# Kernel tuning notes

Measured on AMD Instinct MI355X. Metric: run time of the kernel, lower is better.

The kernel has to match this reference:

```python
import jax, jax.numpy as jnp
import numpy as np

B, C, H, W = 4, 128, 64, 64
E, N, R, K = 256, 16, 8, 4   # d_inner=2C, d_state, dt_rank=ceil(C/16), conv kernel
L = H * W
EPS = 1e-5
NEG_SLOPE = 0.01


def setup_inputs() -> dict:
    key = jax.random.key(0)
    ks = jax.random.split(key, 8)
    p = {}
    p["x"] = jax.random.normal(ks[0], (B, C, H, W), jnp.float32)
    p["bn_gamma"] = jnp.ones((2, C), jnp.float32)
    p["bn_beta"] = jnp.zeros((2, C), jnp.float32)
    p["ln_gamma"] = jnp.ones((2, C), jnp.float32)
    p["ln_beta"] = jnp.zeros((2, C), jnp.float32)
    p["W_in"] = jax.random.normal(ks[1], (2, C, 2 * E), jnp.float32) * 0.02
    p["conv_w"] = jax.random.normal(ks[2], (2, E, K), jnp.float32) * 0.1
    p["conv_b"] = jnp.zeros((2, E), jnp.float32)
    p["W_xp"] = jax.random.normal(ks[3], (2, E, R + 2 * N), jnp.float32) * 0.02
    p["W_dt"] = jax.random.normal(ks[4], (2, R, E), jnp.float32) * 0.1
    # dt bias chosen so softplus(dt) is small/stable (mamba-style init)
    p["b_dt"] = jax.random.uniform(ks[5], (2, E), jnp.float32, minval=-4.0, maxval=-2.0)
    p["A_log"] = jnp.broadcast_to(jnp.log(jnp.arange(1, N + 1, dtype=jnp.float32)), (2, E, N)) + jnp.zeros((2, E, N), jnp.float32)
    p["Dp"] = jnp.ones((2, E), jnp.float32)
    p["W_out"] = jax.random.normal(ks[6], (2, E, C), jnp.float32) * 0.02
    return p


def _stage(x, i, bn_gamma, bn_beta, ln_gamma, ln_beta, W_in, conv_w, conv_b,
           W_xp, W_dt, b_dt, A_log, Dp, W_out):
    # --- BatchNorm2d (batch statistics, biased var, as torch training mode) ---
    mu = x.mean((0, 2, 3))
    var = x.var((0, 2, 3))
    xn = (x - mu[None, :, None, None]) * jax.lax.rsqrt(var + EPS)[None, :, None, None]
    xn = xn * bn_gamma[i][None, :, None, None] + bn_beta[i][None, :, None, None]
    # --- LeakyReLU ---
    xn = jax.nn.leaky_relu(xn, NEG_SLOPE)
    # --- SF_Block (Mamba S6 over L = H*W tokens) ---
    u = xn.transpose(0, 2, 3, 1).reshape(B, L, C)          # [B,L,C] tokens
    mu2 = u.mean(-1, keepdims=True)
    v2 = u.var(-1, keepdims=True)
    un = (u - mu2) * jax.lax.rsqrt(v2 + EPS) * ln_gamma[i] + ln_beta[i]
    xz = un @ W_in[i]                                       # [B,L,2E]
    xm, z = xz[..., :E], xz[..., E:]
    # causal depthwise conv1d along L
    xc = xm.transpose(0, 2, 1)                              # [B,E,L]
    xc = jax.lax.conv_general_dilated(xc, conv_w[i][:, None, :], (1,), [(K - 1, 0)],
                                      feature_group_count=E)
    xm = jax.nn.silu(xc.transpose(0, 2, 1) + conv_b[i])     # [B,L,E]
    dbl = xm @ W_xp[i]                                      # [B,L,R+2N]
    dt = jax.nn.softplus(dbl[..., :R] @ W_dt[i] + b_dt[i])  # [B,L,E]
    Bm = dbl[..., R:R + N]                                  # [B,L,N]
    Cm = dbl[..., R + N:]                                   # [B,L,N]
    A = -jnp.exp(A_log[i])                                  # [E,N]
    dA = jnp.exp(dt[..., None] * A)                         # [B,L,E,N]
    dBx = dt[..., None] * Bm[:, :, None, :] * xm[..., None] # [B,L,E,N]

    def step(h, inp):
        dA_t, dBx_t, C_t = inp
        h = dA_t * h + dBx_t                                # [B,E,N]
        y = jnp.einsum('ben,bn->be', h, C_t)
        return h, y

    h0 = jnp.zeros((B, E, N), xm.dtype)
    _, ys = jax.lax.scan(step, h0, (dA.transpose(1, 0, 2, 3),
                                    dBx.transpose(1, 0, 2, 3),
                                    Cm.transpose(1, 0, 2)))
    y = ys.transpose(1, 0, 2) + Dp[i] * xm                  # skip (D) term
    y = y * jax.nn.silu(z)                                  # gate
    out = y @ W_out[i]                                      # [B,L,C]
    out = u + out                                           # SF residual (drop_path=0)
    return out.reshape(B, H, W, C).transpose(0, 3, 1, 2)


def reference(x, bn_gamma, bn_beta, ln_gamma, ln_beta, W_in, conv_w, conv_b,
              W_xp, W_dt, b_dt, A_log, Dp, W_out):
    residual = x
    out = _stage(x, 0, bn_gamma, bn_beta, ln_gamma, ln_beta, W_in, conv_w, conv_b,
                 W_xp, W_dt, b_dt, A_log, Dp, W_out)
    out = _stage(out, 1, bn_gamma, bn_beta, ln_gamma, ln_beta, W_in, conv_w, conv_b,
                 W_xp, W_dt, b_dt, A_log, Dp, W_out)
    return out + residual
```

## Files before the change

### kernel.cpp

```cpp
#include <hip/hip_runtime.h>
#include <math.h>

#define Bc 4
#define Cc 128
#define Lc 4096
#define Ec 256
#define Nc 16
#define Rc 8
#define Kc 4
#define ROWS (Bc*Lc)
#define EPSc 1e-5f
#define SLOPE 0.01f

#define NCH 128
#define Tc 32
#define SC 16
#define SCL (NCH/SC)

typedef __attribute__((ext_vector_type(8))) short bf16x8;
typedef __attribute__((ext_vector_type(4))) float f32x4;

__device__ inline unsigned pack_bf16_2(float x, float y) {
    unsigned bx = __float_as_uint(x);
    unsigned by = __float_as_uint(y);
    bx = (bx + 0x7FFFu + ((bx >> 16) & 1u)) >> 16;
    by = (by + 0x7FFFu + ((by >> 16) & 1u)) & 0xFFFF0000u;
    return bx | by;
}
__device__ inline unsigned short to_bf16_rne(float x) {
    unsigned b = __float_as_uint(x);
    return (unsigned short)((b + 0x7FFFu + ((b >> 16) & 1u)) >> 16);
}
__device__ inline float bf16f(unsigned short u) {
    return __uint_as_float((unsigned)u << 16);
}
__device__ inline float sigmoidf_fast(float s) {
    return 1.f / (1.f + __expf(-s));
}
__device__ inline float softplusf(float s) {
    return fmaxf(s, 0.f) + __logf(1.f + __expf(-fabsf(s)));
}

__global__ void transpose_in(const float* __restrict__ x, float* __restrict__ xblc) {
    __shared__ float tile[32][33];
    int b = blockIdx.z;
    int l0 = blockIdx.x * 32, c0 = blockIdx.y * 32;
    int tx = threadIdx.x, ty = threadIdx.y;
    tile[ty][tx] = x[((size_t)(b * Cc + c0 + ty)) * Lc + l0 + tx];
    __syncthreads();
    xblc[((size_t)(b * Lc + l0 + ty)) * Cc + c0 + tx] = tile[tx][ty];
}

__device__ inline void wt_one(const float* W, unsigned short* Wt, int idx,
                              int K, int N, int NPAD) {
    int k = idx % K;
    int n = (idx / K) % NPAD;
    int i = idx / (K * NPAD);
    float v = (n < N) ? W[(size_t)i * K * N + (size_t)k * N + n] : 0.f;
    Wt[idx] = to_bf16_rne(v);
}
#define WT1 (2*512*128)
#define WT2 (2*64*256)
#define WT3 (2*128*256)
__global__ void wt_convert_all(const float* __restrict__ W_in, unsigned short* Wt_in,
                               const float* __restrict__ W_xp, unsigned short* Wt_xp,
                               const float* __restrict__ W_out, unsigned short* Wt_out) {
    int idx = blockIdx.x * 256 + threadIdx.x;
    if (idx < WT1) { wt_one(W_in, Wt_in, idx, 128, 512, 512); return; }
    idx -= WT1;
    if (idx < WT2) { wt_one(W_xp, Wt_xp, idx, 256, 40, 64); return; }
    idx -= WT2;
    if (idx < WT3) { wt_one(W_out, Wt_out, idx, 256, 128, 128); }
}

__global__ void bn_stats_partial(const float* __restrict__ xblc, float* __restrict__ part) {
    int c = threadIdx.x;
    int r0 = blockIdx.x * 64;
    float s = 0.f, s2 = 0.f;
    for (int r = 0; r < 64; r++) {
        float v = xblc[(size_t)(r0 + r) * Cc + c];
        s += v; s2 += v * v;
    }
    part[(size_t)blockIdx.x * 256 + c]       = s;
    part[(size_t)blockIdx.x * 256 + 128 + c] = s2;
}
__global__ void bn_stats_final(const float* __restrict__ part, float* __restrict__ sums) {
    int c = threadIdx.x;
    float s = 0.f, s2 = 0.f;
    for (int p = 0; p < 256; p++) {
        s  += part[(size_t)p * 256 + c];
        s2 += part[(size_t)p * 256 + 128 + c];
    }
    sums[c] = s;
    sums[128 + c] = s2;
}

__global__ __launch_bounds__(256) void bn_ln(
        const float* __restrict__ xin, const float* __restrict__ sums,
        const float* __restrict__ bng, const float* __restrict__ bnb,
        const float* __restrict__ lng, const float* __restrict__ lnb,
        float* __restrict__ un) {
    int wave = threadIdx.x >> 6, lane = threadIdx.x & 63;
    int row = blockIdx.x * 4 + wave;
    int c = lane * 2;
    float2 v = *(const float2*)(xin + (size_t)row * Cc + c);
    float2 sm = *(const float2*)(sums + c);
    float2 sq = *(const float2*)(sums + 128 + c);
    float2 g  = *(const float2*)(bng + c);
    float2 bt = *(const float2*)(bnb + c);
    const float inv = 1.f / (float)ROWS;
    float m0 = sm.x * inv, m1 = sm.y * inv;
    float va0 = sq.x * inv - m0 * m0, va1 = sq.y * inv - m1 * m1;
    float xn0 = (v.x - m0) * rsqrtf(va0 + EPSc) * g.x + bt.x;
    float xn1 = (v.y - m1) * rsqrtf(va1 + EPSc) * g.y + bt.y;
    xn0 = (xn0 < 0.f) ? SLOPE * xn0 : xn0;
    xn1 = (xn1 < 0.f) ? SLOPE * xn1 : xn1;
    float s = xn0 + xn1;
    float s2 = xn0 * xn0 + xn1 * xn1;
    #pragma unroll
    for (int m = 1; m < 64; m <<= 1) {
        s  += __shfl_xor(s, m, 64);
        s2 += __shfl_xor(s2, m, 64);
    }
    float m2 = s * (1.f / 128.f);
    float v2 = s2 * (1.f / 128.f) - m2 * m2;
    float rstd = rsqrtf(v2 + EPSc);
    float2 lg = *(const float2*)(lng + c);
    float2 lb = *(const float2*)(lnb + c);
    float2 o;
    o.x = (xn0 - m2) * rstd * lg.x + lb.x;
    o.y = (xn1 - m2) * rstd * lg.y + lb.y;
    *(float2*)(un + (size_t)row * Cc + c) = o;
}

__global__ __launch_bounds__(512) void fused_mid(
        const float* __restrict__ un,
        const unsigned short* __restrict__ Wt_in,
        const float* __restrict__ cw, const float* __restrict__ cb,
        const unsigned short* __restrict__ Wt_xp,
        const float* __restrict__ Wdt, const float* __restrict__ bdt,
        const float* __restrict__ Alog,
        unsigned short* __restrict__ zbuf,
        unsigned* __restrict__ dtxc,
        float* __restrict__ dbl,
        float2* __restrict__ PF) {
    __shared__ __align__(16) unsigned short xmtile[32][Ec + 8];
    __shared__ __align__(16) unsigned short dtt[32][Ec];
    __shared__ unsigned short xmprev[3][Ec];
    __shared__ float dblsh[32][40];
    __shared__ float d8[32][8];
    int tid = threadIdx.x;
    int wave = tid >> 6, lane = tid & 63;
    int quad = lane >> 4, l16 = lane & 15;
    int r0 = blockIdx.x * 32;
    int l0 = r0 & (Lc - 1);

    {
        int rt = wave >> 2;
        int cb4 = (wave & 3) * 8;
        const float* arow = un + (size_t)(r0 + rt * 16 + l16) * Cc + quad * 8;
        bf16x8 af[4];
        #pragma unroll
        for (int s = 0; s < 4; s++) {
            float4 a0 = *(const float4*)(arow + s * 32);
            float4 a1 = *(const float4*)(arow + s * 32 + 4);
            union { unsigned u[4]; bf16x8 v; } t;
            t.u[0] = pack_bf16_2(a0.x, a0.y);
            t.u[1] = pack_bf16_2(a0.z, a0.w);
            t.u[2] = pack_bf16_2(a1.x, a1.y);
            t.u[3] = pack_bf16_2(a1.z, a1.w);
            af[s] = t.v;
        }
        if (l0 != 0) {
            const float* hrow = un + (size_t)(r0 - 16 + l16) * Cc + quad * 8;
            bf16x8 hf[4];
            #pragma unroll
            for (int s = 0; s < 4; s++) {
                float4 a0 = *(const float4*)(hrow + s * 32);
                float4 a1 = *(const float4*)(hrow + s * 32 + 4);
                union { unsigned u[4]; bf16x8 v; } t;
                t.u[0] = pack_bf16_2(a0.x, a0.y);
                t.u[1] = pack_bf16_2(a0.z, a0.w);
                t.u[2] = pack_bf16_2(a1.x, a1.y);
                t.u[3] = pack_bf16_2(a1.z, a1.w);
                hf[s] = t.v;
            }
            #pragma unroll
            for (int c = 0; c < 2; c++) {
                int ct = wave * 2 + c;
                f32x4 acc = f32x4{0, 0, 0, 0};
                const unsigned short* bb = Wt_in + (size_t)(ct * 16 + l16) * Cc + quad * 8;
                #pragma unroll
                for (int s = 0; s < 4; s++)
                    acc = __builtin_amdgcn_mfma_f32_16x16x32_bf16(
                        hf[s], *(const bf16x8*)(bb + s * 32), acc, 0, 0, 0);
                #pragma unroll
                for (int r = 0; r < 4; r++) {
                    int rr = quad * 4 + r;
                    if (rr >= 13) xmprev[rr - 13][ct * 16 + l16] = to_bf16_rne(acc[r]);
                }
            }
        } else {
            for (int idx = tid; idx < 3 * Ec; idx += 512)
                xmprev[idx / Ec][idx % Ec] = 0;
        }
        #pragma unroll
        for (int c = 0; c < 8; c++) {
            int ct = cb4 + c;
            f32x4 acc = f32x4{0, 0, 0, 0};
            const unsigned short* bb = Wt_in + (size_t)(ct * 16 + l16) * Cc + quad * 8;
            #pragma unroll
            for (int s = 0; s < 4; s++)
                acc = __builtin_amdgcn_mfma_f32_16x16x32_bf16(
                    af[s], *(const bf16x8*)(bb + s * 32), acc, 0, 0, 0);
            if (ct < 16) {
                #pragma unroll
                for (int r = 0; r < 4; r++)
                    xmtile[rt * 16 + quad * 4 + r][ct * 16 + l16] = to_bf16_rne(acc[r]);
            } else {
                #pragma unroll
                for (int r = 0; r < 4; r++)
                    zbuf[(size_t)(r0 + rt * 16 + quad * 4 + r) * Ec +
                         (ct - 16) * 16 + l16] = to_bf16_rne(acc[r]);
            }
        }
    }
    __syncthreads();

    int e2 = tid & 255, hh = tid >> 8;
    {
        float pw0, pw1, pw2;
        if (hh == 0) {
            pw0 = bf16f(xmprev[0][e2]);
            pw1 = bf16f(xmprev[1][e2]);
            pw2 = bf16f(xmprev[2][e2]);
        } else {
            pw0 = bf16f(xmtile[13][e2]);
            pw1 = bf16f(xmtile[14][e2]);
            pw2 = bf16f(xmtile[15][e2]);
        }
        __syncthreads();
        float4 w = *(const float4*)(cw + e2 * 4);
        float bias = cb[e2];
        #pragma unroll 4
        for (int k = 0; k < 16; k++) {
            int t = hh * 16 + k;
            float cur = bf16f(xmtile[t][e2]);
            float s = bias + pw0 * w.x + pw1 * w.y + pw2 * w.z + cur * w.w;
            xmtile[t][e2] = to_bf16_rne(s * sigmoidf_fast(s));
            pw0 = pw1; pw1 = pw2; pw2 = cur;
        }
    }
    __syncthreads();

    if (wave < 6) {
        int rt2 = wave & 1, ct2 = wave >> 1;
        bf16x8 a2[8];
        #pragma unroll
        for (int s = 0; s < 8; s++)
            a2[s] = *(const bf16x8*)&xmtile[rt2 * 16 + l16][s * 32 + quad * 8];
        f32x4 acc = f32x4{0, 0, 0, 0};
        const unsigned short* bb = Wt_xp + (size_t)(ct2 * 16 + l16) * Ec + quad * 8;
        #pragma unroll
        for (int s = 0; s < 8; s++)
            acc = __builtin_amdgcn_mfma_f32_16x16x32_bf16(
                a2[s], *(const bf16x8*)(bb + s * 32), acc, 0, 0, 0);
        int col = ct2 * 16 + l16;
        #pragma unroll
        for (int r = 0; r < 4; r++) {
            int row = rt2 * 16 + quad * 4 + r;
            if (col < 40) {
                dblsh[row][col] = acc[r];
                dbl[(size_t)(r0 + row) * 40 + col] = acc[r];
            }
            if (ct2 == 0 && l16 < 8) d8[row][l16] = acc[r];
        }
    }
    __syncthreads();

    {
        float wdt[Rc];
        #pragma unroll
        for (int r = 0; r < Rc; r++) wdt[r] = Wdt[r * Ec + e2];
        float bd = bdt[e2];
        #pragma unroll 4
        for (int k = 0; k < 16; k++) {
            int t = hh * 16 + k;
            float s = bd;
            #pragma unroll
            for (int r = 0; r < Rc; r++) s += d8[t][r] * wdt[r];
            unsigned short db = to_bf16_rne(softplusf(s));
            dtt[t][e2] = db;
            unsigned short xb = xmtile[t][e2];
            dtxc[(size_t)(r0 + t) * Ec + e2] = (unsigned)db | ((unsigned)xb << 16);
        }
    }
    __syncthreads();

    {
        int e = tid >> 1, half = tid & 1;
        float Aen[8];
        #pragma unroll
        for (int n = 0; n < 8; n++) Aen[n] = -__expf(Alog[e * Nc + half * 8 + n]);
        float Pv[8], Fv[8];
        #pragma unroll
        for (int n = 0; n < 8; n++) { Pv[n] = 1.f; Fv[n] = 0.f; }
        for (int t = 0; t < Tc; t++) {
            float dtv = bf16f(dtt[t][e]);
            float xv  = bf16f(xmtile[t][e]);
            float dx = dtv * xv;
            #pragma unroll
            for (int n = 0; n < 8; n++) {
                float dA = __expf(dtv * Aen[n]);
                Pv[n] *= dA;
                Fv[n] = dA * Fv[n] + dx * dblsh[t][8 + half * 8 + n];
            }
        }
        size_t o = ((size_t)blockIdx.x << 12) + tid * 8;
        #pragma unroll
        for (int n = 0; n < 8; n++) PF[o + n] = make_float2(Pv[n], Fv[n]);
    }
}

__global__ void scan_phase2a(const float2* __restrict__ PF, float2* __restrict__ PFS) {
    int idx = blockIdx.x * 256 + threadIdx.x;
    int r = idx & 4095;
    int sc = (idx >> 12) & (SC - 1);
    int b = idx >> 16;
    float Pt = 1.f, Ft = 0.f;
    #pragma unroll
    for (int jj = 0; jj < SCL; jj++) {
        int j = sc * SCL + jj;
        float2 pf = PF[((size_t)(b * NCH + j) << 12) + r];
        Ft = pf.x * Ft + pf.y;
        Pt = pf.x * Pt;
    }
    PFS[((size_t)(b * SC + sc) << 12) + r] = make_float2(Pt, Ft);
}

__global__ void scan_phase2b(float2* PFS) {
    int idx = blockIdx.x * 256 + threadIdx.x;
    int r = idx & 4095;
    int b = idx >> 12;
    float h = 0.f;
    for (int sc = 0; sc < SC; sc++) {
        size_t o = ((size_t)(b * SC + sc) << 12) + r;
        float2 pf = PFS[o];
        PFS[o].x = h;
        h = pf.x * h + pf.y;
    }
}

__global__ void scan_phase2c(float2* __restrict__ PF, const float2* __restrict__ PFS) {
    int idx = blockIdx.x * 256 + threadIdx.x;
    int r = idx & 4095;
    int sc = (idx >> 12) & (SC - 1);
    int b = idx >> 16;
    float h = PFS[((size_t)(b * SC + sc) << 12) + r].x;
    #pragma unroll
    for (int jj = 0; jj < SCL; jj++) {
        int j = sc * SCL + jj;
        size_t o = ((size_t)(b * NCH + j) << 12) + r;
        float2 pf = PF[o];
        PF[o].x = h;
        h = pf.x * h + pf.y;
    }
}

template<int FINAL>
__global__ __launch_bounds__(512) void scan_phase3_out(
        const unsigned* __restrict__ dtxc, const float* __restrict__ dbl,
        const float* __restrict__ Alog,
        const float* __restrict__ Dpv, const float2* __restrict__ PF,
        const unsigned short* __restrict__ zbuf,
        const unsigned short* __restrict__ Wt_out,
        const float* __restrict__ xblc, const float* __restrict__ sums,
        const float* __restrict__ bng, const float* __restrict__ bnb,
        const float* __restrict__ xorig, float* __restrict__ outp) {
    __shared__ __align__(16) unsigned dtxc_sh[32][Ec];
    __shared__ __align__(16) unsigned short zytile[Tc][Ec + 8];
    __shared__ float Bsh[Tc][Nc];
    __shared__ float Csh[Tc][Nc];
    int blk = blockIdx.x;
    int b = blk >> 7, j = blk & (NCH - 1);
    int tid = threadIdx.x;
    int e = tid >> 1, half = tid & 1;
    int base_row = b * Lc + j * Tc;
    {
        const uint4* src = (const uint4*)(dtxc + (size_t)base_row * Ec);
        uint4* dst = (uint4*)&dtxc_sh[0][0];
        #pragma unroll
        for (int k = 0; k < 4; k++) dst[tid + k * 512] = src[tid + k * 512];
        const uint4* zsrc = (const uint4*)(zbuf + (size_t)base_row * Ec);
        #pragma unroll
        for (int k = 0; k < 2; k++) {
            int idx = tid + k * 512;
            int row = idx >> 5, c8 = idx & 31;
            *(uint4*)&zytile[row][c8 * 8] = zsrc[idx];
        }
        int t = tid >> 4, n = tid & 15;
        Bsh[t][n] = dbl[(size_t)(base_row + t) * 40 + 8 + n];
        Csh[t][n] = dbl[(size_t)(base_row + t) * 40 + 24 + n];
    }
    __syncthreads();
    float Aen[8];
    #pragma unroll
    for (int n = 0; n < 8; n++) Aen[n] = -__expf(Alog[e * Nc + half * 8 + n]);
    float h[8];
    size_t o = ((size_t)blk << 12) + tid * 8;
    #pragma unroll
    for (int n = 0; n < 8; n++) h[n] = PF[o + n].x;
    float dp = Dpv[e];
    for (int t = 0; t < Tc; t++) {
        unsigned pk = dtxc_sh[t][e];
        float dtv = __uint_as_float(pk << 16);
        float xv  = __uint_as_float(pk & 0xFFFF0000u);
        float dx = dtv * xv;
        float acc = 0.f;
        #pragma unroll
        for (int n = 0; n < 8; n++) {
            float dA = __expf(dtv * Aen[n]);
            h[n] = dA * h[n] + dx * Bsh[t][half * 8 + n];
            acc += h[n] * Csh[t][half * 8 + n];
        }
        acc += __shfl_xor(acc, 1, 64);
        if (half == 0) {
            float yv = acc + dp * xv;
            float zv = bf16f(zytile[t][e]);
            zytile[t][e] = to_bf16_rne(yv * (zv * sigmoidf_fast(zv)));
        }
    }
    __syncthreads();

    int wave = tid >> 6, lane = tid & 63;
    int quad = lane >> 4, l16 = lane & 15;
    int col = wave * 16 + l16;
    const unsigned short* bb = Wt_out + (size_t)col * Ec + quad * 8;
    const float inv = 1.f / (float)ROWS;
    float mean = sums[col] * inv;
    float var  = sums[128 + col] * inv - mean * mean;
    float rstdg = rsqrtf(var + EPSc) * bng[col];
    float bbeta = bnb[col];
    #pragma unroll
    for (int rt = 0; rt < 2; rt++) {
        f32x4 acc = f32x4{0, 0, 0, 0};
        #pragma unroll
        for (int s = 0; s < 8; s++) {
            bf16x8 af = *(const bf16x8*)&zytile[rt * 16 + l16][s * 32 + quad * 8];
            acc = __builtin_amdgcn_mfma_f32_16x16x32_bf16(
                af, *(const bf16x8*)(bb + s * 32), acc, 0, 0, 0);
        }
        int row0 = base_row + rt * 16 + quad * 4;
        if (FINAL) {
            int l = row0 & (Lc - 1);
            size_t tb = ((size_t)(b * Cc + col) << 12) + l;
            float4 xo = *(const float4*)(xorig + tb);
            float4 res;
            #pragma unroll
            for (int r = 0; r < 4; r++) {
                float xb = xblc[(size_t)(row0 + r) * Cc + col];
                float xn = (xb - mean) * rstdg + bbeta;
                float uv = (xn < 0.f) ? SLOPE * xn : xn;
                ((float*)&res)[r] = acc[r] + uv + ((const float*)&xo)[r];
            }
            *(float4*)(outp + tb) = res;
        } else {
            #pragma unroll
            for (int r = 0; r < 4; r++) {
                int row = row0 + r;
                float xb = xblc[(size_t)row * Cc + col];
                float xn = (xb - mean) * rstdg + bbeta;
                float uv = (xn < 0.f) ? SLOPE * xn : xn;
                outp[(size_t)row * Cc + col] = acc[r] + uv;
            }
        }
    }
}

extern "C" void kernel_launch(void* const* d_in, const int* in_sizes, int n_in,
                              void* d_out, int out_size, void* d_ws, size_t ws_size,
                              hipStream_t stream) {
    const float* x        = (const float*)d_in[0];
    const float* bn_gamma = (const float*)d_in[1];
    const float* bn_beta  = (const float*)d_in[2];
    const float* ln_gamma = (const float*)d_in[3];
    const float* ln_beta  = (const float*)d_in[4];
    const float* W_in     = (const float*)d_in[5];
    const float* conv_w   = (const float*)d_in[6];
    const float* conv_b   = (const float*)d_in[7];
    const float* W_xp     = (const float*)d_in[8];
    const float* W_dt     = (const float*)d_in[9];
    const float* b_dt     = (const float*)d_in[10];
    const float* A_log    = (const float*)d_in[11];
    const float* Dp       = (const float*)d_in[12];
    const float* W_out    = (const float*)d_in[13];
    float* out = (float*)d_out;

    char* ws = (char*)d_ws;
    size_t off = 0;
    auto alloc = [&](size_t nbytes) {
        char* p = ws + off;
        off += ((nbytes + 255) / 256) * 256;
        return p;
    };
    float* xblc = (float*)alloc((size_t)ROWS * Cc * 4);
    float* un   = (float*)alloc((size_t)ROWS * Cc * 4);
    unsigned short* zbuf = (unsigned short*)alloc((size_t)ROWS * Ec * 2);
    unsigned* dtxc = (unsigned*)alloc((size_t)ROWS * Ec * 4);
    float* dbl  = (float*)alloc((size_t)ROWS * 40 * 4);
    float2* PF  = (float2*)alloc((size_t)Bc * NCH * Ec * Nc * 8);
    float2* PFS = (float2*)alloc((size_t)Bc * SC * Ec * Nc * 8);
    float* part = (float*)alloc(256 * 256 * 4);
    float* sums = (float*)alloc(256 * 4);
    unsigned short* Wt_in  = (unsigned short*)alloc((size_t)WT1 * 2);
    unsigned short* Wt_xp  = (unsigned short*)alloc((size_t)WT2 * 2);
    unsigned short* Wt_out = (unsigned short*)alloc((size_t)WT3 * 2);

    transpose_in<<<dim3(Lc / 32, Cc / 32, Bc), dim3(32, 32), 0, stream>>>(x, xblc);
    wt_convert_all<<<(WT1 + WT2 + WT3) / 256, 256, 0, stream>>>(
        W_in, Wt_in, W_xp, Wt_xp, W_out, Wt_out);

    for (int i = 0; i < 2; i++) {
        bn_stats_partial<<<256, 128, 0, stream>>>(xblc, part);
        bn_stats_final<<<1, 128, 0, stream>>>(part, sums);
        bn_ln<<<ROWS / 4, 256, 0, stream>>>(xblc, sums,
                                            bn_gamma + i * Cc, bn_beta + i * Cc,
                                            ln_gamma + i * Cc, ln_beta + i * Cc, un);
        fused_mid<<<ROWS / 32, 512, 0, stream>>>(
            un, Wt_in + (size_t)i * 512 * 128,
            conv_w + i * Ec * Kc, conv_b + i * Ec,
            Wt_xp + (size_t)i * 64 * 256,
            W_dt + i * Rc * Ec, b_dt + i * Ec, A_log + i * Ec * Nc,
            zbuf, dtxc, dbl, PF);
        scan_phase2a<<<(Bc * SC * 4096) / 256, 256, 0, stream>>>(PF, PFS);
        scan_phase2b<<<(Bc * 4096) / 256, 256, 0, stream>>>(PFS);
        scan_phase2c<<<(Bc * SC * 4096) / 256, 256, 0, stream>>>(PF, PFS);
        if (i == 0) {
            scan_phase3_out<0><<<Bc * NCH, 512, 0, stream>>>(
                dtxc, dbl, A_log + i * Ec * Nc, Dp + i * Ec, PF,
                zbuf, Wt_out + (size_t)i * 128 * 256,
                xblc, sums, bn_gamma + i * Cc, bn_beta + i * Cc,
                nullptr, xblc);
        } else {
            scan_phase3_out<1><<<Bc * NCH, 512, 0, stream>>>(
                dtxc, dbl, A_log + i * Ec * Nc, Dp + i * Ec, PF,
                zbuf, Wt_out + (size_t)i * 128 * 256,
                xblc, sums, bn_gamma + i * Cc, bn_beta + i * Cc,
                x, out);
        }
    }
}
```

Measured before the change: 311.1 us.

## Double block size of fused_mid and scan_phase3 to 1024 threads, splitting state dims four ways

Raises fused_mid and scan_phase3_out from 512 to 1024 threads per block. The work is redistributed so each thread handles 4 of the 16 state dimensions instead of 8, conv and dt rows are split into 8-row slices, and GEMM column tiles are spread across more waves. It also stores the packed dt/x word in shared memory so the scan reads a single value. The aim is more parallelism per chunk and shorter per-thread serial chains. In exchange it adds an extra shuffle reduction, a tighter register budget from launch_bounds(1024,8), and possibly lower occupancy.

```diff
diff --git a/kernel.cpp b/kernel.cpp
--- a/kernel.cpp
+++ b/kernel.cpp
@@ -133,7 +133,7 @@
     *(float2*)(un + (size_t)row * Cc + c) = o;
 }
 
-__global__ __launch_bounds__(512) void fused_mid(
+__global__ __launch_bounds__(1024, 8) void fused_mid(
         const float* __restrict__ un,
         const unsigned short* __restrict__ Wt_in,
         const float* __restrict__ cw, const float* __restrict__ cb,
@@ -145,7 +145,7 @@
         float* __restrict__ dbl,
         float2* __restrict__ PF) {
     __shared__ __align__(16) unsigned short xmtile[32][Ec + 8];
-    __shared__ __align__(16) unsigned short dtt[32][Ec];
+    __shared__ __align__(16) unsigned dtpk[32][Ec];
     __shared__ unsigned short xmprev[3][Ec];
     __shared__ float dblsh[32][40];
     __shared__ float d8[32][8];
@@ -156,21 +156,6 @@
     int l0 = r0 & (Lc - 1);
 
     {
-        int rt = wave >> 2;
-        int cb4 = (wave & 3) * 8;
-        const float* arow = un + (size_t)(r0 + rt * 16 + l16) * Cc + quad * 8;
-        bf16x8 af[4];
-        #pragma unroll
-        for (int s = 0; s < 4; s++) {
-            float4 a0 = *(const float4*)(arow + s * 32);
-            float4 a1 = *(const float4*)(arow + s * 32 + 4);
-            union { unsigned u[4]; bf16x8 v; } t;
-            t.u[0] = pack_bf16_2(a0.x, a0.y);
-            t.u[1] = pack_bf16_2(a0.z, a0.w);
-            t.u[2] = pack_bf16_2(a1.x, a1.y);
-            t.u[3] = pack_bf16_2(a1.z, a1.w);
-            af[s] = t.v;
-        }
         if (l0 != 0) {
             const float* hrow = un + (size_t)(r0 - 16 + l16) * Cc + quad * 8;
             bf16x8 hf[4];
@@ -185,27 +170,38 @@
                 t.u[3] = pack_bf16_2(a1.z, a1.w);
                 hf[s] = t.v;
             }
+            int ct = wave;
+            f32x4 acc = f32x4{0, 0, 0, 0};
+            const unsigned short* bb = Wt_in + (size_t)(ct * 16 + l16) * Cc + quad * 8;
             #pragma unroll
-            for (int c = 0; c < 2; c++) {
-                int ct = wave * 2 + c;
-                f32x4 acc = f32x4{0, 0, 0, 0};
-                const unsigned short* bb = Wt_in + (size_t)(ct * 16 + l16) * Cc + quad * 8;
-                #pragma unroll
-                for (int s = 0; s < 4; s++)
-                    acc = __builtin_amdgcn_mfma_f32_16x16x32_bf16(
-                        hf[s], *(const bf16x8*)(bb + s * 32), acc, 0, 0, 0);
-                #pragma unroll
-                for (int r = 0; r < 4; r++) {
-                    int rr = quad * 4 + r;
-                    if (rr >= 13) xmprev[rr - 13][ct * 16 + l16] = to_bf16_rne(acc[r]);
-                }
+            for (int s = 0; s < 4; s++)
+                acc = __builtin_amdgcn_mfma_f32_16x16x32_bf16(
+                    hf[s], *(const bf16x8*)(bb + s * 32), acc, 0, 0, 0);
+            #pragma unroll
+            for (int r = 0; r < 4; r++) {
+                int rr = quad * 4 + r;
+                if (rr >= 13) xmprev[rr - 13][ct * 16 + l16] = to_bf16_rne(acc[r]);
             }
         } else {
-            for (int idx = tid; idx < 3 * Ec; idx += 512)
-                xmprev[idx / Ec][idx % Ec] = 0;
-        }
-        #pragma unroll
-        for (int c = 0; c < 8; c++) {
+            if (tid < 3 * Ec) xmprev[tid / Ec][tid % Ec] = 0;
+        }
+        int rt = wave >> 3;
+        int cb4 = (wave & 7) * 4;
+        const float* arow = un + (size_t)(r0 + rt * 16 + l16) * Cc + quad * 8;
+        bf16x8 af[4];
+        #pragma unroll
+        for (int s = 0; s < 4; s++) {
+            float4 a0 = *(const float4*)(arow + s * 32);
+            float4 a1 = *(const float4*)(arow + s * 32 + 4);
+            union { unsigned u[4]; bf16x8 v; } t;
+            t.u[0] = pack_bf16_2(a0.x, a0.y);
+            t.u[1] = pack_bf16_2(a0.z, a0.w);
+            t.u[2] = pack_bf16_2(a1.x, a1.y);
+            t.u[3] = pack_bf16_2(a1.z, a1.w);
+            af[s] = t.v;
+        }
+        #pragma unroll
+        for (int c = 0; c < 4; c++) {
             int ct = cb4 + c;
             f32x4 acc = f32x4{0, 0, 0, 0};
             const unsigned short* bb = Wt_in + (size_t)(ct * 16 + l16) * Cc + quad * 8;
@@ -235,16 +231,16 @@
             pw1 = bf16f(xmprev[1][e2]);
             pw2 = bf16f(xmprev[2][e2]);
         } else {
-            pw0 = bf16f(xmtile[13][e2]);
-            pw1 = bf16f(xmtile[14][e2]);
-            pw2 = bf16f(xmtile[15][e2]);
+            pw0 = bf16f(xmtile[hh * 8 - 3][e2]);
+            pw1 = bf16f(xmtile[hh * 8 - 2][e2]);
+            pw2 = bf16f(xmtile[hh * 8 - 1][e2]);
         }
         __syncthreads();
         float4 w = *(const float4*)(cw + e2 * 4);
         float bias = cb[e2];
-        #pragma unroll 4
-        for (int k = 0; k < 16; k++) {
-            int t = hh * 16 + k;
+        #pragma unroll
+        for (int k = 0; k < 8; k++) {
+            int t = hh * 8 + k;
             float cur = bf16f(xmtile[t][e2]);
             float s = bias + pw0 * w.x + pw1 * w.y + pw2 * w.z + cur * w.w;
             xmtile[t][e2] = to_bf16_rne(s * sigmoidf_fast(s));
@@ -283,42 +279,43 @@
         #pragma unroll
         for (int r = 0; r < Rc; r++) wdt[r] = Wdt[r * Ec + e2];
         float bd = bdt[e2];
-        #pragma unroll 4
-        for (int k = 0; k < 16; k++) {
-            int t = hh * 16 + k;
+        #pragma unroll
+        for (int k = 0; k < 8; k++) {
+            int t = hh * 8 + k;
             float s = bd;
             #pragma unroll
             for (int r = 0; r < Rc; r++) s += d8[t][r] * wdt[r];
             unsigned short db = to_bf16_rne(softplusf(s));
-            dtt[t][e2] = db;
-            unsigned short xb = xmtile[t][e2];
-            dtxc[(size_t)(r0 + t) * Ec + e2] = (unsigned)db | ((unsigned)xb << 16);
+            unsigned pk = (unsigned)db | ((unsigned)xmtile[t][e2] << 16);
+            dtpk[t][e2] = pk;
+            dtxc[(size_t)(r0 + t) * Ec + e2] = pk;
         }
     }
     __syncthreads();
 
     {
-        int e = tid >> 1, half = tid & 1;
-        float Aen[8];
-        #pragma unroll
-        for (int n = 0; n < 8; n++) Aen[n] = -__expf(Alog[e * Nc + half * 8 + n]);
-        float Pv[8], Fv[8];
-        #pragma unroll
-        for (int n = 0; n < 8; n++) { Pv[n] = 1.f; Fv[n] = 0.f; }
+        int e = tid >> 2, q = tid & 3;
+        float Aen[4];
+        #pragma unroll
+        for (int n = 0; n < 4; n++) Aen[n] = -__expf(Alog[e * Nc + q * 4 + n]);
+        float Pv[4], Fv[4];
+        #pragma unroll
+        for (int n = 0; n < 4; n++) { Pv[n] = 1.f; Fv[n] = 0.f; }
         for (int t = 0; t < Tc; t++) {
-            float dtv = bf16f(dtt[t][e]);
-            float xv  = bf16f(xmtile[t][e]);
+            unsigned pk = dtpk[t][e];
+            float dtv = __uint_as_float(pk << 16);
+            float xv  = __uint_as_float(pk & 0xFFFF0000u);
             float dx = dtv * xv;
             #pragma unroll
-            for (int n = 0; n < 8; n++) {
+            for (int n = 0; n < 4; n++) {
                 float dA = __expf(dtv * Aen[n]);
                 Pv[n] *= dA;
-                Fv[n] = dA * Fv[n] + dx * dblsh[t][8 + half * 8 + n];
+                Fv[n] = dA * Fv[n] + dx * dblsh[t][8 + q * 4 + n];
             }
         }
-        size_t o = ((size_t)blockIdx.x << 12) + tid * 8;
-        #pragma unroll
-        for (int n = 0; n < 8; n++) PF[o + n] = make_float2(Pv[n], Fv[n]);
+        size_t o = ((size_t)blockIdx.x << 12) + tid * 4;
+        #pragma unroll
+        for (int n = 0; n < 4; n++) PF[o + n] = make_float2(Pv[n], Fv[n]);
     }
 }
 
@@ -368,7 +365,7 @@
 }
 
 template<int FINAL>
-__global__ __launch_bounds__(512) void scan_phase3_out(
+__global__ __launch_bounds__(1024, 8) void scan_phase3_out(
         const unsigned* __restrict__ dtxc, const float* __restrict__ dbl,
         const float* __restrict__ Alog,
         const float* __restrict__ Dpv, const float2* __restrict__ PF,
@@ -384,32 +381,32 @@
     int blk = blockIdx.x;
     int b = blk >> 7, j = blk & (NCH - 1);
     int tid = threadIdx.x;
-    int e = tid >> 1, half = tid & 1;
     int base_row = b * Lc + j * Tc;
     {
         const uint4* src = (const uint4*)(dtxc + (size_t)base_row * Ec);
         uint4* dst = (uint4*)&dtxc_sh[0][0];
-        #pragma unroll
-        for (int k = 0; k < 4; k++) dst[tid + k * 512] = src[tid + k * 512];
+        dst[tid] = src[tid];
+        dst[tid + 1024] = src[tid + 1024];
         const uint4* zsrc = (const uint4*)(zbuf + (size_t)base_row * Ec);
-        #pragma unroll
-        for (int k = 0; k < 2; k++) {
-            int idx = tid + k * 512;
-            int row = idx >> 5, c8 = idx & 31;
-            *(uint4*)&zytile[row][c8 * 8] = zsrc[idx];
-        }
-        int t = tid >> 4, n = tid & 15;
-        Bsh[t][n] = dbl[(size_t)(base_row + t) * 40 + 8 + n];
-        Csh[t][n] = dbl[(size_t)(base_row + t) * 40 + 24 + n];
-    }
-    __syncthreads();
-    float Aen[8];
+        {
+            int row = tid >> 5, c8 = tid & 31;
+            *(uint4*)&zytile[row][c8 * 8] = zsrc[tid];
+        }
+        if (tid < 512) {
+            int t = tid >> 4, n = tid & 15;
+            Bsh[t][n] = dbl[(size_t)(base_row + t) * 40 + 8 + n];
+            Csh[t][n] = dbl[(size_t)(base_row + t) * 40 + 24 + n];
+        }
+    }
+    __syncthreads();
+    int e = tid >> 2, q = tid & 3;
+    float Aen[4];
     #pragma unroll
-    for (int n = 0; n < 8; n++) Aen[n] = -__expf(Alog[e * Nc + half * 8 + n]);
-    float h[8];
-    size_t o = ((size_t)blk << 12) + tid * 8;
+    for (int n = 0; n < 4; n++) Aen[n] = -__expf(Alog[e * Nc + q * 4 + n]);
+    float h[4];
+    size_t o = ((size_t)blk << 12) + tid * 4;
     #pragma unroll
-    for (int n = 0; n < 8; n++) h[n] = PF[o + n].x;
+    for (int n = 0; n < 4; n++) h[n] = PF[o + n].x;
     float dp = Dpv[e];
     for (int t = 0; t < Tc; t++) {
         unsigned pk = dtxc_sh[t][e];
@@ -418,13 +415,14 @@
         float dx = dtv * xv;
         float acc = 0.f;
         #pragma unroll
-        for (int n = 0; n < 8; n++) {
+        for (int n = 0; n < 4; n++) {
             float dA = __expf(dtv * Aen[n]);
-            h[n] = dA * h[n] + dx * Bsh[t][half * 8 + n];
-            acc += h[n] * Csh[t][half * 8 + n];
+            h[n] = dA * h[n] + dx * Bsh[t][q * 4 + n];
+            acc += h[n] * Csh[t][q * 4 + n];
         }
         acc += __shfl_xor(acc, 1, 64);
-        if (half == 0) {
+        acc += __shfl_xor(acc, 2, 64);
+        if (q == 0) {
             float yv = acc + dp * xv;
             float zv = bf16f(zytile[t][e]);
             zytile[t][e] = to_bf16_rne(yv * (zv * sigmoidf_fast(zv)));
@@ -434,45 +432,43 @@
 
     int wave = tid >> 6, lane = tid & 63;
     int quad = lane >> 4, l16 = lane & 15;
-    int col = wave * 16 + l16;
+    int rt = wave & 1, c8 = wave >> 1;
+    int col = c8 * 16 + l16;
     const unsigned short* bb = Wt_out + (size_t)col * Ec + quad * 8;
     const float inv = 1.f / (float)ROWS;
     float mean = sums[col] * inv;
     float var  = sums[128 + col] * inv - mean * mean;
     float rstdg = rsqrtf(var + EPSc) * bng[col];
     float bbeta = bnb[col];
+    f32x4 acc = f32x4{0, 0, 0, 0};
     #pragma unroll
-    for (int rt = 0; rt < 2; rt++) {
-        f32x4 acc = f32x4{0, 0, 0, 0};
-        #pragma unroll
-        for (int s = 0; s < 8; s++) {
-            bf16x8 af = *(const bf16x8*)&zytile[rt * 16 + l16][s * 32 + quad * 8];
-            acc = __builtin_amdgcn_mfma_f32_16x16x32_bf16(
-                af, *(const bf16x8*)(bb + s * 32), acc, 0, 0, 0);
-        }
-        int row0 = base_row + rt * 16 + quad * 4;
-        if (FINAL) {
-            int l = row0 & (Lc - 1);
-            size_t tb = ((size_t)(b * Cc + col) << 12) + l;
-            float4 xo = *(const float4*)(xorig + tb);
-            float4 res;
-            #pragma unroll
-            for (int r = 0; r < 4; r++) {
-                float xb = xblc[(size_t)(row0 + r) * Cc + col];
-                float xn = (xb - mean) * rstdg + bbeta;
-                float uv = (xn < 0.f) ? SLOPE * xn : xn;
-                ((float*)&res)[r] = acc[r] + uv + ((const float*)&xo)[r];
-            }
-            *(float4*)(outp + tb) = res;
-        } else {
-            #pragma unroll
-            for (int r = 0; r < 4; r++) {
-                int row = row0 + r;
-                float xb = xblc[(size_t)row * Cc + col];
-                float xn = (xb - mean) * rstdg + bbeta;
-                float uv = (xn < 0.f) ? SLOPE * xn : xn;
-                outp[(size_t)row * Cc + col] = acc[r] + uv;
-            }
+    for (int s = 0; s < 8; s++) {
+        bf16x8 af = *(const bf16x8*)&zytile[rt * 16 + l16][s * 32 + quad * 8];
+        acc = __builtin_amdgcn_mfma_f32_16x16x32_bf16(
+            af, *(const bf16x8*)(bb + s * 32), acc, 0, 0, 0);
+    }
+    int row0 = base_row + rt * 16 + quad * 4;
+    if (FINAL) {
+        int l = row0 & (Lc - 1);
+        size_t tb = ((size_t)(b * Cc + col) << 12) + l;
+        float4 xo = *(const float4*)(xorig + tb);
+        float4 res;
+        #pragma unroll
+        for (int r = 0; r < 4; r++) {
+            float xb = xblc[(size_t)(row0 + r) * Cc + col];
+            float xn = (xb - mean) * rstdg + bbeta;
+            float uv = (xn < 0.f) ? SLOPE * xn : xn;
+            ((float*)&res)[r] = acc[r] + uv + ((const float*)&xo)[r];
+        }
+        *(float4*)(outp + tb) = res;
+    } else {
+        #pragma unroll
+        for (int r = 0; r < 4; r++) {
+            int row = row0 + r;
+            float xb = xblc[(size_t)row * Cc + col];
+            float xn = (xb - mean) * rstdg + bbeta;
+            float uv = (xn < 0.f) ? SLOPE * xn : xn;
+            outp[(size_t)row * Cc + col] = acc[r] + uv;
         }
     }
 }
@@ -526,7 +522,7 @@
         bn_ln<<<ROWS / 4, 256, 0, stream>>>(xblc, sums,
                                             bn_gamma + i * Cc, bn_beta + i * Cc,
                                             ln_gamma + i * Cc, ln_beta + i * Cc, un);
-        fused_mid<<<ROWS / 32, 512, 0, stream>>>(
+        fused_mid<<<ROWS / 32, 1024, 0, stream>>>(
             un, Wt_in + (size_t)i * 512 * 128,
             conv_w + i * Ec * Kc, conv_b + i * Ec,
             Wt_xp + (size_t)i * 64 * 256,
@@ -536,13 +532,13 @@
         scan_phase2b<<<(Bc * 4096) / 256, 256, 0, stream>>>(PFS);
         scan_phase2c<<<(Bc * SC * 4096) / 256, 256, 0, stream>>>(PF, PFS);
         if (i == 0) {
-            scan_phase3_out<0><<<Bc * NCH, 512, 0, stream>>>(
+            scan_phase3_out<0><<<Bc * NCH, 1024, 0, stream>>>(
                 dtxc, dbl, A_log + i * Ec * Nc, Dp + i * Ec, PF,
                 zbuf, Wt_out + (size_t)i * 128 * 256,
                 xblc, sums, bn_gamma + i * Cc, bn_beta + i * Cc,
                 nullptr, xblc);
         } else {
-            scan_phase3_out<1><<<Bc * NCH, 512, 0, stream>>>(
+            scan_phase3_out<1><<<Bc * NCH, 1024, 0, stream>>>(
                 dtxc, dbl, A_log + i * Ec * Nc, Dp + i * Ec, PF,
                 zbuf, Wt_out + (size_t)i * 128 * 256,
                 xblc, sums, bn_gamma + i * Cc, bn_beta + i * Cc,
```

Result: slower. 336.7 us (+8.2%).

## Recompute z in scan output kernel, fuse BN stats via atomics, drop scan phase2c

Applied to the files above, without the earlier changes.

The z half of the input projection is no longer written to a bf16 global buffer. It is recomputed with MFMA inside the scan output kernel from the normalized activations. The separate phase-2c prefix propagation kernel is removed: each chunk block rebuilds its starting state from the super-chunk prefix plus up to three preceding chunk transfer factors, with super-chunk count doubled to keep that walk short. BatchNorm statistics for the second stage are accumulated with atomics in the first stage's output epilogue, and the first stage uses a single atomic stats kernel, removing the partial/final reduction launches. This trades extra MFMA work and PF reads per block for fewer launches and less global traffic, and atomic float sums make the statistics order-nondeterministic.

```diff
diff --git a/kernel.cpp b/kernel.cpp
--- a/kernel.cpp
+++ b/kernel.cpp
@@ -14,7 +14,7 @@
 
 #define NCH 128
 #define Tc 32
-#define SC 16
+#define SC 32
 #define SCL (NCH/SC)
 
 typedef __attribute__((ext_vector_type(8))) short bf16x8;
@@ -73,7 +73,7 @@
     if (idx < WT3) { wt_one(W_out, Wt_out, idx, 256, 128, 128); }
 }
 
-__global__ void bn_stats_partial(const float* __restrict__ xblc, float* __restrict__ part) {
+__global__ void bn_stats_atomic(const float* __restrict__ xblc, float* __restrict__ sums) {
     int c = threadIdx.x;
     int r0 = blockIdx.x * 64;
     float s = 0.f, s2 = 0.f;
@@ -81,18 +81,8 @@
         float v = xblc[(size_t)(r0 + r) * Cc + c];
         s += v; s2 += v * v;
     }
-    part[(size_t)blockIdx.x * 256 + c]       = s;
-    part[(size_t)blockIdx.x * 256 + 128 + c] = s2;
-}
-__global__ void bn_stats_final(const float* __restrict__ part, float* __restrict__ sums) {
-    int c = threadIdx.x;
-    float s = 0.f, s2 = 0.f;
-    for (int p = 0; p < 256; p++) {
-        s  += part[(size_t)p * 256 + c];
-        s2 += part[(size_t)p * 256 + 128 + c];
-    }
-    sums[c] = s;
-    sums[128 + c] = s2;
+    atomicAdd(sums + c, s);
+    atomicAdd(sums + 128 + c, s2);
 }
 
 __global__ __launch_bounds__(256) void bn_ln(
@@ -140,12 +130,11 @@
         const unsigned short* __restrict__ Wt_xp,
         const float* __restrict__ Wdt, const float* __restrict__ bdt,
         const float* __restrict__ Alog,
-        unsigned short* __restrict__ zbuf,
         unsigned* __restrict__ dtxc,
         float* __restrict__ dbl,
         float2* __restrict__ PF) {
     __shared__ __align__(16) unsigned short xmtile[32][Ec + 8];
-    __shared__ __align__(16) unsigned short dtt[32][Ec];
+    __shared__ __align__(16) unsigned dtpk[32][Ec];
     __shared__ unsigned short xmprev[3][Ec];
     __shared__ float dblsh[32][40];
     __shared__ float d8[32][8];
@@ -156,21 +145,6 @@
     int l0 = r0 & (Lc - 1);
 
     {
-        int rt = wave >> 2;
-        int cb4 = (wave & 3) * 8;
-        const float* arow = un + (size_t)(r0 + rt * 16 + l16) * Cc + quad * 8;
-        bf16x8 af[4];
-        #pragma unroll
-        for (int s = 0; s < 4; s++) {
-            float4 a0 = *(const float4*)(arow + s * 32);
-            float4 a1 = *(const float4*)(arow + s * 32 + 4);
-            union { unsigned u[4]; bf16x8 v; } t;
-            t.u[0] = pack_bf16_2(a0.x, a0.y);
-            t.u[1] = pack_bf16_2(a0.z, a0.w);
-            t.u[2] = pack_bf16_2(a1.x, a1.y);
-            t.u[3] = pack_bf16_2(a1.z, a1.w);
-            af[s] = t.v;
-        }
         if (l0 != 0) {
             const float* hrow = un + (size_t)(r0 - 16 + l16) * Cc + quad * 8;
             bf16x8 hf[4];
@@ -204,8 +178,23 @@
             for (int idx = tid; idx < 3 * Ec; idx += 512)
                 xmprev[idx / Ec][idx % Ec] = 0;
         }
-        #pragma unroll
-        for (int c = 0; c < 8; c++) {
+        int rt = wave & 1;
+        int cb4 = (wave >> 1) * 4;
+        const float* arow = un + (size_t)(r0 + rt * 16 + l16) * Cc + quad * 8;
+        bf16x8 af[4];
+        #pragma unroll
+        for (int s = 0; s < 4; s++) {
+            float4 a0 = *(const float4*)(arow + s * 32);
+            float4 a1 = *(const float4*)(arow + s * 32 + 4);
+            union { unsigned u[4]; bf16x8 v; } t;
+            t.u[0] = pack_bf16_2(a0.x, a0.y);
+            t.u[1] = pack_bf16_2(a0.z, a0.w);
+            t.u[2] = pack_bf16_2(a1.x, a1.y);
+            t.u[3] = pack_bf16_2(a1.z, a1.w);
+            af[s] = t.v;
+        }
+        #pragma unroll
+        for (int c = 0; c < 4; c++) {
             int ct = cb4 + c;
             f32x4 acc = f32x4{0, 0, 0, 0};
             const unsigned short* bb = Wt_in + (size_t)(ct * 16 + l16) * Cc + quad * 8;
@@ -213,16 +202,9 @@
             for (int s = 0; s < 4; s++)
                 acc = __builtin_amdgcn_mfma_f32_16x16x32_bf16(
                     af[s], *(const bf16x8*)(bb + s * 32), acc, 0, 0, 0);
-            if (ct < 16) {
-                #pragma unroll
-                for (int r = 0; r < 4; r++)
-                    xmtile[rt * 16 + quad * 4 + r][ct * 16 + l16] = to_bf16_rne(acc[r]);
-            } else {
-                #pragma unroll
-                for (int r = 0; r < 4; r++)
-                    zbuf[(size_t)(r0 + rt * 16 + quad * 4 + r) * Ec +
-                         (ct - 16) * 16 + l16] = to_bf16_rne(acc[r]);
-            }
+            #pragma unroll
+            for (int r = 0; r < 4; r++)
+                xmtile[rt * 16 + quad * 4 + r][ct * 16 + l16] = to_bf16_rne(acc[r]);
         }
     }
     __syncthreads();
@@ -290,9 +272,9 @@
             #pragma unroll
             for (int r = 0; r < Rc; r++) s += d8[t][r] * wdt[r];
             unsigned short db = to_bf16_rne(softplusf(s));
-            dtt[t][e2] = db;
-            unsigned short xb = xmtile[t][e2];
-            dtxc[(size_t)(r0 + t) * Ec + e2] = (unsigned)db | ((unsigned)xb << 16);
+            unsigned pk = (unsigned)db | ((unsigned)xmtile[t][e2] << 16);
+            dtpk[t][e2] = pk;
+            dtxc[(size_t)(r0 + t) * Ec + e2] = pk;
         }
     }
     __syncthreads();
@@ -306,8 +288,9 @@
         #pragma unroll
         for (int n = 0; n < 8; n++) { Pv[n] = 1.f; Fv[n] = 0.f; }
         for (int t = 0; t < Tc; t++) {
-            float dtv = bf16f(dtt[t][e]);
-            float xv  = bf16f(xmtile[t][e]);
+            unsigned pk = dtpk[t][e];
+            float dtv = __uint_as_float(pk << 16);
+            float xv  = __uint_as_float(pk & 0xFFFF0000u);
             float dx = dtv * xv;
             #pragma unroll
             for (int n = 0; n < 8; n++) {
@@ -326,7 +309,7 @@
     int idx = blockIdx.x * 256 + threadIdx.x;
     int r = idx & 4095;
     int sc = (idx >> 12) & (SC - 1);
-    int b = idx >> 16;
+    int b = idx >> 17;
     float Pt = 1.f, Ft = 0.f;
     #pragma unroll
     for (int jj = 0; jj < SCL; jj++) {
@@ -351,89 +334,115 @@
     }
 }
 
-__global__ void scan_phase2c(float2* __restrict__ PF, const float2* __restrict__ PFS) {
-    int idx = blockIdx.x * 256 + threadIdx.x;
-    int r = idx & 4095;
-    int sc = (idx >> 12) & (SC - 1);
-    int b = idx >> 16;
-    float h = PFS[((size_t)(b * SC + sc) << 12) + r].x;
-    #pragma unroll
-    for (int jj = 0; jj < SCL; jj++) {
-        int j = sc * SCL + jj;
-        size_t o = ((size_t)(b * NCH + j) << 12) + r;
-        float2 pf = PF[o];
-        PF[o].x = h;
-        h = pf.x * h + pf.y;
-    }
-}
-
 template<int FINAL>
 __global__ __launch_bounds__(512) void scan_phase3_out(
         const unsigned* __restrict__ dtxc, const float* __restrict__ dbl,
         const float* __restrict__ Alog,
         const float* __restrict__ Dpv, const float2* __restrict__ PF,
-        const unsigned short* __restrict__ zbuf,
+        const float2* __restrict__ PFS,
+        const float* __restrict__ un, const unsigned short* __restrict__ Wt_in,
         const unsigned short* __restrict__ Wt_out,
         const float* __restrict__ xblc, const float* __restrict__ sums,
         const float* __restrict__ bng, const float* __restrict__ bnb,
+        float* __restrict__ sums_next,
         const float* __restrict__ xorig, float* __restrict__ outp) {
     __shared__ __align__(16) unsigned dtxc_sh[32][Ec];
-    __shared__ __align__(16) unsigned short zytile[Tc][Ec + 8];
+    __shared__ __align__(16) unsigned short zsh[Tc][Ec + 8];
     __shared__ float Bsh[Tc][Nc];
     __shared__ float Csh[Tc][Nc];
     int blk = blockIdx.x;
     int b = blk >> 7, j = blk & (NCH - 1);
     int tid = threadIdx.x;
-    int e = tid >> 1, half = tid & 1;
+    int wave = tid >> 6, lane = tid & 63;
+    int quad = lane >> 4, l16 = lane & 15;
     int base_row = b * Lc + j * Tc;
+
     {
         const uint4* src = (const uint4*)(dtxc + (size_t)base_row * Ec);
         uint4* dst = (uint4*)&dtxc_sh[0][0];
         #pragma unroll
         for (int k = 0; k < 4; k++) dst[tid + k * 512] = src[tid + k * 512];
-        const uint4* zsrc = (const uint4*)(zbuf + (size_t)base_row * Ec);
-        #pragma unroll
-        for (int k = 0; k < 2; k++) {
-            int idx = tid + k * 512;
-            int row = idx >> 5, c8 = idx & 31;
-            *(uint4*)&zytile[row][c8 * 8] = zsrc[idx];
-        }
         int t = tid >> 4, n = tid & 15;
         Bsh[t][n] = dbl[(size_t)(base_row + t) * 40 + 8 + n];
         Csh[t][n] = dbl[(size_t)(base_row + t) * 40 + 24 + n];
     }
-    __syncthreads();
-    float Aen[8];
-    #pragma unroll
-    for (int n = 0; n < 8; n++) Aen[n] = -__expf(Alog[e * Nc + half * 8 + n]);
     float h[8];
-    size_t o = ((size_t)blk << 12) + tid * 8;
-    #pragma unroll
-    for (int n = 0; n < 8; n++) h[n] = PF[o + n].x;
-    float dp = Dpv[e];
-    for (int t = 0; t < Tc; t++) {
-        unsigned pk = dtxc_sh[t][e];
-        float dtv = __uint_as_float(pk << 16);
-        float xv  = __uint_as_float(pk & 0xFFFF0000u);
-        float dx = dtv * xv;
-        float acc = 0.f;
-        #pragma unroll
-        for (int n = 0; n < 8; n++) {
-            float dA = __expf(dtv * Aen[n]);
-            h[n] = dA * h[n] + dx * Bsh[t][half * 8 + n];
-            acc += h[n] * Csh[t][half * 8 + n];
-        }
-        acc += __shfl_xor(acc, 1, 64);
-        if (half == 0) {
-            float yv = acc + dp * xv;
-            float zv = bf16f(zytile[t][e]);
-            zytile[t][e] = to_bf16_rne(yv * (zv * sigmoidf_fast(zv)));
-        }
-    }
-    __syncthreads();
-
-    int wave = tid >> 6, lane = tid & 63;
-    int quad = lane >> 4, l16 = lane & 15;
+    {
+        int sc = j >> 2, m = j & 3;
+        size_t rb = tid * 8;
+        size_t os = (((size_t)(b * SC + sc)) << 12) + rb;
+        #pragma unroll
+        for (int n = 0; n < 8; n++) h[n] = PFS[os + n].x;
+        for (int jj = 0; jj < m; jj++) {
+            size_t oc = (((size_t)(b * NCH + sc * 4 + jj)) << 12) + rb;
+            #pragma unroll
+            for (int n = 0; n < 8; n++) {
+                float2 pf = PF[oc + n];
+                h[n] = pf.x * h[n] + pf.y;
+            }
+        }
+    }
+    {
+        int rt = wave & 1;
+        int cb4 = (wave >> 1) * 4;
+        const float* arow = un + (size_t)(base_row + rt * 16 + l16) * Cc + quad * 8;
+        bf16x8 af[4];
+        #pragma unroll
+        for (int s = 0; s < 4; s++) {
+            float4 a0 = *(const float4*)(arow + s * 32);
+            float4 a1 = *(const float4*)(arow + s * 32 + 4);
+            union { unsigned u[4]; bf16x8 v; } t;
+            t.u[0] = pack_bf16_2(a0.x, a0.y);
+            t.u[1] = pack_bf16_2(a0.z, a0.w);
+            t.u[2] = pack_bf16_2(a1.x, a1.y);
+            t.u[3] = pack_bf16_2(a1.z, a1.w);
+            af[s] = t.v;
+        }
+        #pragma unroll
+        for (int c = 0; c < 4; c++) {
+            int ct = cb4 + c;
+            f32x4 acc = f32x4{0, 0, 0, 0};
+            const unsigned short* bb =
+                Wt_in + (size_t)(256 + ct * 16 + l16) * Cc + quad * 8;
+            #pragma unroll
+            for (int s = 0; s < 4; s++)
+                acc = __builtin_amdgcn_mfma_f32_16x16x32_bf16(
+                    af[s], *(const bf16x8*)(bb + s * 32), acc, 0, 0, 0);
+            #pragma unroll
+            for (int r = 0; r < 4; r++)
+                zsh[rt * 16 + quad * 4 + r][ct * 16 + l16] = to_bf16_rne(acc[r]);
+        }
+    }
+    __syncthreads();
+
+    int e = tid >> 1, half = tid & 1;
+    {
+        float Aen[8];
+        #pragma unroll
+        for (int n = 0; n < 8; n++) Aen[n] = -__expf(Alog[e * Nc + half * 8 + n]);
+        float dp = Dpv[e];
+        for (int t = 0; t < Tc; t++) {
+            unsigned pk = dtxc_sh[t][e];
+            float dtv = __uint_as_float(pk << 16);
+            float xv  = __uint_as_float(pk & 0xFFFF0000u);
+            float dx = dtv * xv;
+            float acc = 0.f;
+            #pragma unroll
+            for (int n = 0; n < 8; n++) {
+                float dA = __expf(dtv * Aen[n]);
+                h[n] = dA * h[n] + dx * Bsh[t][half * 8 + n];
+                acc += h[n] * Csh[t][half * 8 + n];
+            }
+            acc += __shfl_xor(acc, 1, 64);
+            if (half == 0) {
+                float yv = acc + dp * xv;
+                float zv = bf16f(zsh[t][e]);
+                zsh[t][e] = to_bf16_rne(yv * (zv * sigmoidf_fast(zv)));
+            }
+        }
+    }
+    __syncthreads();
+
     int col = wave * 16 + l16;
     const unsigned short* bb = Wt_out + (size_t)col * Ec + quad * 8;
     const float inv = 1.f / (float)ROWS;
@@ -441,12 +450,13 @@
     float var  = sums[128 + col] * inv - mean * mean;
     float rstdg = rsqrtf(var + EPSc) * bng[col];
     float bbeta = bnb[col];
+    float ls = 0.f, lq = 0.f;
     #pragma unroll
     for (int rt = 0; rt < 2; rt++) {
         f32x4 acc = f32x4{0, 0, 0, 0};
         #pragma unroll
         for (int s = 0; s < 8; s++) {
-            bf16x8 af = *(const bf16x8*)&zytile[rt * 16 + l16][s * 32 + quad * 8];
+            bf16x8 af = *(const bf16x8*)&zsh[rt * 16 + l16][s * 32 + quad * 8];
             acc = __builtin_amdgcn_mfma_f32_16x16x32_bf16(
                 af, *(const bf16x8*)(bb + s * 32), acc, 0, 0, 0);
         }
@@ -471,8 +481,20 @@
                 float xb = xblc[(size_t)row * Cc + col];
                 float xn = (xb - mean) * rstdg + bbeta;
                 float uv = (xn < 0.f) ? SLOPE * xn : xn;
-                outp[(size_t)row * Cc + col] = acc[r] + uv;
-            }
+                float v = acc[r] + uv;
+                outp[(size_t)row * Cc + col] = v;
+                ls += v; lq += v * v;
+            }
+        }
+    }
+    if (!FINAL) {
+        ls += __shfl_xor(ls, 16, 64);
+        ls += __shfl_xor(ls, 32, 64);
+        lq += __shfl_xor(lq, 16, 64);
+        lq += __shfl_xor(lq, 32, 64);
+        if (quad == 0) {
+            atomicAdd(sums_next + col, ls);
+            atomicAdd(sums_next + 128 + col, lq);
         }
     }
 }
@@ -505,25 +527,24 @@
     };
     float* xblc = (float*)alloc((size_t)ROWS * Cc * 4);
     float* un   = (float*)alloc((size_t)ROWS * Cc * 4);
-    unsigned short* zbuf = (unsigned short*)alloc((size_t)ROWS * Ec * 2);
     unsigned* dtxc = (unsigned*)alloc((size_t)ROWS * Ec * 4);
     float* dbl  = (float*)alloc((size_t)ROWS * 40 * 4);
     float2* PF  = (float2*)alloc((size_t)Bc * NCH * Ec * Nc * 8);
     float2* PFS = (float2*)alloc((size_t)Bc * SC * Ec * Nc * 8);
-    float* part = (float*)alloc(256 * 256 * 4);
-    float* sums = (float*)alloc(256 * 4);
+    float* sums = (float*)alloc(512 * 4);
     unsigned short* Wt_in  = (unsigned short*)alloc((size_t)WT1 * 2);
     unsigned short* Wt_xp  = (unsigned short*)alloc((size_t)WT2 * 2);
     unsigned short* Wt_out = (unsigned short*)alloc((size_t)WT3 * 2);
 
+    hipMemsetAsync(sums, 0, 512 * sizeof(float), stream);
     transpose_in<<<dim3(Lc / 32, Cc / 32, Bc), dim3(32, 32), 0, stream>>>(x, xblc);
     wt_convert_all<<<(WT1 + WT2 + WT3) / 256, 256, 0, stream>>>(
         W_in, Wt_in, W_xp, Wt_xp, W_out, Wt_out);
+    bn_stats_atomic<<<256, 128, 0, stream>>>(xblc, sums);
 
     for (int i = 0; i < 2; i++) {
-        bn_stats_partial<<<256, 128, 0, stream>>>(xblc, part);
-        bn_stats_final<<<1, 128, 0, stream>>>(part, sums);
-        bn_ln<<<ROWS / 4, 256, 0, stream>>>(xblc, sums,
+        float* sums_i = sums + i * 256;
+        bn_ln<<<ROWS / 4, 256, 0, stream>>>(xblc, sums_i,
                                             bn_gamma + i * Cc, bn_beta + i * Cc,
                                             ln_gamma + i * Cc, ln_beta + i * Cc, un);
         fused_mid<<<ROWS / 32, 512, 0, stream>>>(
@@ -531,22 +552,23 @@
             conv_w + i * Ec * Kc, conv_b + i * Ec,
             Wt_xp + (size_t)i * 64 * 256,
             W_dt + i * Rc * Ec, b_dt + i * Ec, A_log + i * Ec * Nc,
-            zbuf, dtxc, dbl, PF);
+            dtxc, dbl, PF);
         scan_phase2a<<<(Bc * SC * 4096) / 256, 256, 0, stream>>>(PF, PFS);
         scan_phase2b<<<(Bc * 4096) / 256, 256, 0, stream>>>(PFS);
-        scan_phase2c<<<(Bc * SC * 4096) / 256, 256, 0, stream>>>(PF, PFS);
         if (i == 0) {
             scan_phase3_out<0><<<Bc * NCH, 512, 0, stream>>>(
-                dtxc, dbl, A_log + i * Ec * Nc, Dp + i * Ec, PF,
-                zbuf, Wt_out + (size_t)i * 128 * 256,
-                xblc, sums, bn_gamma + i * Cc, bn_beta + i * Cc,
-                nullptr, xblc);
+                dtxc, dbl, A_log + i * Ec * Nc, Dp + i * Ec, PF, PFS,
+                un, Wt_in + (size_t)i * 512 * 128,
+                Wt_out + (size_t)i * 128 * 256,
+                xblc, sums_i, bn_gamma + i * Cc, bn_beta + i * Cc,
+                sums + 256, nullptr, xblc);
         } else {
             scan_phase3_out<1><<<Bc * NCH, 512, 0, stream>>>(
-                dtxc, dbl, A_log + i * Ec * Nc, Dp + i * Ec, PF,
-                zbuf, Wt_out + (size_t)i * 128 * 256,
-                xblc, sums, bn_gamma + i * Cc, bn_beta + i * Cc,
-                x, out);
-        }
-    }
-}
+                dtxc, dbl, A_log + i * Ec * Nc, Dp + i * Ec, PF, PFS,
+                un, Wt_in + (size_t)i * 512 * 128,
+                Wt_out + (size_t)i * 128 * 256,
+                xblc, sums_i, bn_gamma + i * Cc, bn_beta + i * Cc,
+                nullptr, x, out);
+        }
+    }
+}
```

Result: faster. 302.2 us (-2.9%).
